# Performance work log

Hardware: AMD Instinct MI355X
Metric: run time of the kernel (lower is better)

Reference implementation:

```python
import jax, jax.numpy as jnp
import numpy as np

B, S, D, H = 4, 2048, 1024, 16
DK = D // H
THETA = 10000.0


def apply_rope(x, pos, theta):
    # x: [B, H, S, DK], pos: [S] int
    d = x.shape[-1]
    inv_freq = theta ** (-jnp.arange(0, d, 2, dtype=jnp.float32) / d)  # [d/2]
    ang = pos.astype(jnp.float32)[:, None] * inv_freq[None, :]          # [S, d/2]
    cos, sin = jnp.cos(ang), jnp.sin(ang)
    x1 = x[..., 0::2]
    x2 = x[..., 1::2]
    r1 = x1 * cos - x2 * sin
    r2 = x1 * sin + x2 * cos
    return jnp.stack([r1, r2], axis=-1).reshape(x.shape)


def setup_inputs() -> dict:
    key = jax.random.key(0)
    ks = jax.random.split(key, 5)
    scale = 1.0 / np.sqrt(D)
    x = jax.random.normal(ks[0], (B, S, D), dtype=jnp.float32)
    Wq = jax.random.normal(ks[1], (D, D), dtype=jnp.float32) * scale
    Wk = jax.random.normal(ks[2], (D, D), dtype=jnp.float32) * scale
    Wv = jax.random.normal(ks[3], (D, D), dtype=jnp.float32) * scale
    Wo = jax.random.normal(ks[4], (D, D), dtype=jnp.float32) * scale
    token_positions = jnp.arange(S, dtype=jnp.int32)
    return {"x": x, "token_positions": token_positions,
            "Wq": Wq, "Wk": Wk, "Wv": Wv, "Wo": Wo}


def reference(x, token_positions, Wq, Wk, Wv, Wo):
    b, s, d = x.shape
    # Linear (no bias), weight stored [out, in]: y = x @ W.T
    q = (x @ Wq.T).reshape(b, s, H, DK).transpose(0, 2, 1, 3)  # [B,H,S,DK]
    k = (x @ Wk.T).reshape(b, s, H, DK).transpose(0, 2, 1, 3)
    v = (x @ Wv.T).reshape(b, s, H, DK).transpose(0, 2, 1, 3)
    q = apply_rope(q, token_positions, THETA)
    k = apply_rope(k, token_positions, THETA)
    scores = jnp.einsum('bhqd,bhkd->bhqk', q, k) / jnp.sqrt(jnp.float32(DK))
    causal = jnp.tril(jnp.ones((s, s), dtype=bool))
    scores = jnp.where(causal, scores, -jnp.inf)
    attn = jax.nn.softmax(scores, axis=-1)
    out = jnp.einsum('bhqk,bhkd->bhqd', attn, v)
    out = out.transpose(0, 2, 1, 3).reshape(b, s, d)
    return out @ Wo.T
```

## Files before the change

### kernel.cpp

```cpp
#include <hip/hip_runtime.h>

typedef unsigned short u16;
typedef __bf16 bf16x8 __attribute__((ext_vector_type(8)));
typedef float f32x4 __attribute__((ext_vector_type(4)));
typedef u16 u16x8 __attribute__((ext_vector_type(8)));
typedef u16 u16x4 __attribute__((ext_vector_type(4)));
typedef short s16x4 __attribute__((ext_vector_type(4)));

union V8 { u16x8 u; bf16x8 b; };
union V4 { u16x4 u; s16x4 s; unsigned w[2]; };

#define NB 4
#define NS 2048
#define ND 1024
#define NH 16
#define NDK 64
#define LP 80
#define CP 136
#define QSCL 0.18033688011112042f
#define FMAX 20.0f

__device__ __forceinline__ u16 f2bf(float f) {
  union { float f; unsigned u; } v; v.f = f;
  return (u16)((v.u + 0x7fffu + ((v.u >> 16) & 1u)) >> 16);
}

__device__ __forceinline__ unsigned pk2bf(float a, float b) {
#if __has_builtin(__builtin_amdgcn_cvt_pk_bf16_f32)
  auto v = __builtin_amdgcn_cvt_pk_bf16_f32(a, b);
  unsigned r; __builtin_memcpy(&r, &v, 4);
  return r;
#else
  return (unsigned)f2bf(a) | ((unsigned)f2bf(b) << 16);
#endif
}

__device__ __forceinline__ float fexp2(float x) {
#if __has_builtin(__builtin_amdgcn_exp2f)
  return __builtin_amdgcn_exp2f(x);
#else
  return exp2f(x);
#endif
}

__device__ __forceinline__ bf16x8 lds_frag(const u16* p) {
  V8 t; t.u = *(const u16x8*)p; return t.b;
}

__global__ __launch_bounds__(256) void cvt_bf16(const float* __restrict__ s,
                                                u16* __restrict__ d, int n) {
  const int i = (blockIdx.x * 256 + threadIdx.x) * 8;
  if (i >= n) return;
  const f32x4 lo = *(const f32x4*)(s + i);
  const f32x4 hi = *(const f32x4*)(s + i + 4);
  union { unsigned w[4]; u16x8 v; } o;
  o.w[0] = pk2bf(lo[0], lo[1]);
  o.w[1] = pk2bf(lo[2], lo[3]);
  o.w[2] = pk2bf(hi[0], hi[1]);
  o.w[3] = pk2bf(hi[2], hi[3]);
  *(u16x8*)(d + i) = o.v;
}

__global__ __launch_bounds__(256) void cvt_w4(const float* __restrict__ w0,
                                              const float* __restrict__ w1,
                                              const float* __restrict__ w2,
                                              const float* __restrict__ w3,
                                              u16* __restrict__ d) {
  const float* s = (blockIdx.y == 0) ? w0 : (blockIdx.y == 1) ? w1
                 : (blockIdx.y == 2) ? w2 : w3;
  const int i = (blockIdx.x * 256 + threadIdx.x) * 8;
  const f32x4 lo = *(const f32x4*)(s + i);
  const f32x4 hi = *(const f32x4*)(s + i + 4);
  union { unsigned w[4]; u16x8 v; } o;
  o.w[0] = pk2bf(lo[0], lo[1]);
  o.w[1] = pk2bf(lo[2], lo[3]);
  o.w[2] = pk2bf(hi[0], hi[1]);
  o.w[3] = pk2bf(hi[2], hi[3]);
  *(u16x8*)(d + (size_t)blockIdx.y * ND * ND + i) = o.v;
}

__global__ __launch_bounds__(256) void rope_tbl(const int* __restrict__ tp,
                                                float2* __restrict__ tbl) {
  const int i = blockIdx.x * 256 + threadIdx.x;
  const int s = i >> 5, d = i & 31;
  const float inv = __expf(-(float)d * 0.28782313662425572f);
  const float ang = (float)tp[s] * inv;
  float sn, cs;
  __sincosf(ang, &sn, &cs);
  tbl[i] = make_float2(cs, sn);
}

__global__ __launch_bounds__(256) void gemm_qkv(
    const u16* __restrict__ X, const u16* __restrict__ W0,
    const u16* __restrict__ W1, const u16* __restrict__ W2,
    void* __restrict__ O0, void* __restrict__ O1, void* __restrict__ O2,
    const float2* __restrict__ tbl, int modebase) {
  __shared__ u16 smem[2 * 128 * LP];
  u16* ldsA = smem;
  u16* ldsB = smem + 128 * LP;
  const int tid = threadIdx.x;
  const int lane = tid & 63;
  const int w = tid >> 6;
  const int quad = lane >> 4;
  const int l15 = lane & 15;
  const int z = blockIdx.z;
  const u16* Wp = (z == 0) ? W0 : (z == 1) ? W1 : W2;
  void* Op = (z == 0) ? O0 : (z == 1) ? O1 : O2;
  const int mode = modebase + z;
  const int m0 = blockIdx.x * 128;
  const int n0 = blockIdx.y * 128;
  const int wm = (w >> 1) * 64;
  const int wn = (w & 1) * 64;

  const int srow = tid >> 3;
  const int scol = (tid & 7) * 8;
  const u16* Ag = X + (size_t)(m0 + srow) * ND + scol;
  const u16* Bg = Wp + (size_t)(n0 + srow) * ND + scol;

  f32x4 acc[4][4];
  const f32x4 z4 = {0.f, 0.f, 0.f, 0.f};
  for (int i = 0; i < 4; i++)
    for (int j = 0; j < 4; j++) acc[i][j] = z4;

  for (int k0 = 0; k0 < ND; k0 += 64) {
    u16x8 ar[4], br[4];
    for (int r = 0; r < 4; r++) {
      ar[r] = *(const u16x8*)(Ag + (size_t)r * 32 * ND + k0);
      br[r] = *(const u16x8*)(Bg + (size_t)r * 32 * ND + k0);
    }
    __syncthreads();
    for (int r = 0; r < 4; r++) {
      *(u16x8*)&ldsA[(r * 32 + srow) * LP + scol] = ar[r];
      *(u16x8*)&ldsB[(r * 32 + srow) * LP + scol] = br[r];
    }
    __syncthreads();
    for (int kk = 0; kk < 2; kk++) {
      bf16x8 af[4], bfr[4];
      for (int mt = 0; mt < 4; mt++)
        af[mt] = lds_frag(&ldsA[(wm + mt * 16 + l15) * LP + (kk * 4 + quad) * 8]);
      for (int nt = 0; nt < 4; nt++)
        bfr[nt] = lds_frag(&ldsB[(wn + nt * 16 + l15) * LP + (kk * 4 + quad) * 8]);
      for (int mt = 0; mt < 4; mt++)
        for (int nt = 0; nt < 4; nt++)
          acc[mt][nt] = __builtin_amdgcn_mfma_f32_16x16x32_bf16(
              af[mt], bfr[nt], acc[mt][nt], 0, 0, 0);
    }
  }
  __syncthreads();

  if (mode < 2) {
    u16* cb = smem;
    for (int nt = 0; nt < 4; nt++) {
      const int n_g = n0 + wn + nt * 16 + l15;
      const int dk = n_g & 63;
      const float sgn = (dk & 1) ? 1.f : -1.f;
      const int d2 = dk >> 1;
      for (int mt = 0; mt < 4; mt++) {
        const int mrow = wm + mt * 16 + quad * 4;
        for (int r = 0; r < 4; r++) {
          const int m_g = m0 + mrow + r;
          float v = acc[mt][nt][r];
          const int s_i = m_g & (NS - 1);
          const float partner = __shfl_xor(v, 1);
          const float2 t = tbl[s_i * 32 + d2];
          v = v * t.x + partner * t.y * sgn;
          if (mode == 0) v *= QSCL;
          cb[(mrow + r) * CP + wn + nt * 16 + l15] = f2bf(v);
        }
      }
    }
    __syncthreads();
    const int c = (tid & 15) * 8;
    const int h = (n0 + c) >> 6;
    const int dk0 = (n0 + c) & 63;
    for (int p = 0; p < 8; p++) {
      const int row = p * 16 + (tid >> 4);
      const int m_g = m0 + row;
      const int b = m_g >> 11;
      const int s_i = m_g & (NS - 1);
      *(u16x8*)&((u16*)Op)[(size_t)(((b * NH) + h) * NS + s_i) * NDK + dk0] =
          *(const u16x8*)&cb[row * CP + c];
    }
  } else if (mode == 2) {
    u16* cbT = smem;
    for (int nt = 0; nt < 4; nt++)
      for (int mt = 0; mt < 4; mt++)
        for (int r = 0; r < 4; r++)
          cbT[(wn + nt * 16 + l15) * CP + wm + mt * 16 + quad * 4 + r] =
              f2bf(acc[mt][nt][r]);
    __syncthreads();
    const int b = m0 >> 11;
    const int s0 = m0 & (NS - 1);
    const int col = (tid & 15) * 8;
    for (int p = 0; p < 8; p++) {
      const int row = p * 16 + (tid >> 4);
      const int dkg = n0 + row;
      const int h = dkg >> 6;
      *(u16x8*)&((u16*)Op)[(size_t)(((b * NH) + h) * NDK + (dkg & 63)) * NS +
                           s0 + col] = *(const u16x8*)&cbT[row * CP + col];
    }
  } else {
    for (int nt = 0; nt < 4; nt++) {
      const int n_g = n0 + wn + nt * 16 + l15;
      for (int mt = 0; mt < 4; mt++) {
        const int mb = m0 + wm + mt * 16 + quad * 4;
        for (int r = 0; r < 4; r++)
          ((float*)Op)[(size_t)(mb + r) * ND + n_g] = acc[mt][nt][r];
      }
    }
  }
}

__global__ __launch_bounds__(512, 4) void attn(const u16* __restrict__ Q,
                                               const u16* __restrict__ Kc,
                                               const u16* __restrict__ Vt,
                                               u16* __restrict__ AO,
                                               unsigned* __restrict__ ctr) {
  __shared__ u16 smem[2 * 64 * LP];
  u16* kt = smem;
  u16* vt = smem + 64 * LP;
  __shared__ unsigned s_item;
  const int tid = threadIdx.x;
  const int lane = tid & 63;
  const int w = tid >> 6;
  const int quad = lane >> 4;
  const int l15 = lane & 15;

  if (tid == 0) s_item = atomicAdd(ctr, 1u) & 1023u;
  __syncthreads();
  const unsigned item = s_item;
  const int qt = 15 - (int)(item >> 6);
  const int bh = (int)(item & 63u);
  const int q0 = qt * 128;
  const int qg = q0 + w * 16 + l15;
  const int qmin = q0 + w * 16;

  const int x7 = l15 & 7;
  const int kb0 = l15 * LP + ((quad ^ x7) * 8);
  const int kb1 = l15 * LP + (((4 + quad) ^ x7) * 8);
  int vb[4];
#pragma unroll
  for (int nt = 0; nt < 4; nt++)
    vb[nt] = l15 * LP + (((2 * nt + (quad >> 1)) ^ x7) * 8) + 4 * (quad & 1);
  const int srow = tid >> 3;
  const int sg = tid & 7;
  const int woff = srow * LP + ((sg ^ (srow & 7)) * 8);

  const u16* Qb = Q + (size_t)bh * NS * NDK + (size_t)qg * NDK + quad * 8;
  const bf16x8 qf0 = lds_frag(Qb);
  const bf16x8 qf1 = lds_frag(Qb + 32);

  f32x4 oacc[4];
  const f32x4 z4 = {0.f, 0.f, 0.f, 0.f};
#pragma unroll
  for (int i = 0; i < 4; i++) oacc[i] = z4;
  float ls0 = 0.f, ls1 = 0.f;

  const u16* Kb = Kc + (size_t)bh * NS * NDK;
  const u16* Vg = Vt + (size_t)bh * NDK * NS;

  u16x8 kreg = *(const u16x8*)(Kb + (size_t)srow * NDK + sg * 8);
  u16x8 vreg = *(const u16x8*)(Vg + (size_t)srow * NS + sg * 8);

  const int jend = q0 + 64;
  const f32x4 nF = {-FMAX, -FMAX, -FMAX, -FMAX};
  for (int j0 = 0; j0 <= jend; j0 += 64) {
    __syncthreads();
    *(u16x8*)&kt[woff] = kreg;
    *(u16x8*)&vt[woff] = vreg;
    __syncthreads();
    if (j0 + 64 <= jend) {
      const int nj = j0 + 64;
      kreg = *(const u16x8*)(Kb + (size_t)(nj + srow) * NDK + sg * 8);
      vreg = *(const u16x8*)(Vg + (size_t)srow * NS + nj + sg * 8);
    }

    if (j0 <= qmin + 15) {
      f32x4 sa[4];
#pragma unroll
      for (int i = 0; i < 4; i++) sa[i] = nF;
      __builtin_amdgcn_s_setprio(1);
#pragma unroll
      for (int nt = 0; nt < 4; nt++) {
        const bf16x8 kf0 = lds_frag(&kt[kb0 + nt * (16 * LP)]);
        sa[nt] = __builtin_amdgcn_mfma_f32_16x16x32_bf16(kf0, qf0, sa[nt], 0, 0, 0);
      }
#pragma unroll
      for (int nt = 0; nt < 4; nt++) {
        const bf16x8 kf1 = lds_frag(&kt[kb1 + nt * (16 * LP)]);
        sa[nt] = __builtin_amdgcn_mfma_f32_16x16x32_bf16(kf1, qf1, sa[nt], 0, 0, 0);
      }
      __builtin_amdgcn_s_setprio(0);

      const bool domask = (j0 + 63 > qmin);
      s16x4 pa[4];
#pragma unroll
      for (int nt = 0; nt < 4; nt++) {
        float p0 = fexp2(sa[nt][0]);
        float p1 = fexp2(sa[nt][1]);
        float p2 = fexp2(sa[nt][2]);
        float p3 = fexp2(sa[nt][3]);
        if (domask) {
          const int kbase = j0 + nt * 16 + quad * 4;
          if (kbase + 0 > qg) p0 = 0.f;
          if (kbase + 1 > qg) p1 = 0.f;
          if (kbase + 2 > qg) p2 = 0.f;
          if (kbase + 3 > qg) p3 = 0.f;
        }
        ls0 += p0 + p1;
        ls1 += p2 + p3;
        V4 t;
        t.w[0] = pk2bf(p0, p1);
        t.w[1] = pk2bf(p2, p3);
        pa[nt] = t.s;
      }

      __builtin_amdgcn_s_setprio(1);
#pragma unroll
      for (int dt = 0; dt < 4; dt++) {
#pragma unroll
        for (int nt = 0; nt < 4; nt++) {
          V4 t;
          t.u = *(const u16x4*)&vt[vb[nt] + dt * (16 * LP)];
          oacc[dt] = __builtin_amdgcn_mfma_f32_16x16x16bf16_1k(pa[nt], t.s,
                                                               oacc[dt], 0, 0, 0);
        }
      }
      __builtin_amdgcn_s_setprio(0);
    }
  }

  float lsum = ls0 + ls1;
  lsum += __shfl_xor(lsum, 16);
  lsum += __shfl_xor(lsum, 32);
  float lq[4];
#pragma unroll
  for (int r = 0; r < 4; r++) lq[r] = __shfl(lsum, quad * 4 + r);

  __syncthreads();
  u16* ob = smem;
#pragma unroll
  for (int dt = 0; dt < 4; dt++)
#pragma unroll
    for (int r = 0; r < 4; r++)
      ob[(w * 16 + quad * 4 + r) * 72 + dt * 16 + l15] =
          f2bf(oacc[dt][r] / lq[r]);
  __syncthreads();
  const int b = bh >> 4, h = bh & 15;
#pragma unroll
  for (int p2 = 0; p2 < 2; p2++) {
    const int idx = p2 * 512 + tid;
    const int row = idx >> 3;
    const int c = (idx & 7) * 8;
    *(u16x8*)&AO[(size_t)(b * NS + q0 + row) * ND + h * 64 + c] =
        *(const u16x8*)&ob[row * 72 + c];
  }
}

extern "C" void kernel_launch(void* const* d_in, const int* in_sizes, int n_in,
                              void* d_out, int out_size, void* d_ws, size_t ws_size,
                              hipStream_t stream) {
  const float* x = (const float*)d_in[0];
  const int* tp = (const int*)d_in[1];
  const float* Wq = (const float*)d_in[2];
  const float* Wk = (const float*)d_in[3];
  const float* Wv = (const float*)d_in[4];
  const float* Wo = (const float*)d_in[5];

  const size_t NE = (size_t)NB * NS * ND;
  const int NW = ND * ND;
  u16* Qb = (u16*)d_ws;
  u16* Kb = Qb + NE;
  u16* Vtb = Kb + NE;
  u16* Xbf = Vtb + NE;
  u16* Wbf = Xbf + NE;
  u16* wend = Wbf + 4 * (size_t)NW;
  unsigned* ctr = (unsigned*)wend;
  float2* tbl = (float2*)(wend + 8);

  dim3 blk(256);
  cvt_bf16<<<dim3((unsigned)(NE / 2048)), blk, 0, stream>>>(x, Xbf, (int)NE);
  cvt_w4<<<dim3(NW / 2048, 4), blk, 0, stream>>>(Wq, Wk, Wv, Wo, Wbf);
  rope_tbl<<<dim3(256), blk, 0, stream>>>(tp, tbl);
  gemm_qkv<<<dim3(64, 8, 3), blk, 0, stream>>>(
      Xbf, Wbf, Wbf + (size_t)NW, Wbf + 2 * (size_t)NW, Qb, Kb, Vtb, tbl, 0);
  attn<<<dim3(1024), dim3(512), 0, stream>>>(Qb, Kb, Vtb, Xbf, ctr);
  gemm_qkv<<<dim3(64, 8, 1), blk, 0, stream>>>(
      Xbf, Wbf + 3 * (size_t)NW, Wbf + 3 * (size_t)NW, Wbf + 3 * (size_t)NW,
      d_out, d_out, d_out, tbl, 3);
}
```

Measured before the change: 281.9 us.

## Shrink attention blocks to 64-query tiles and drop atomic work counter

The attention kernel now uses 256-thread blocks handling 64 queries each (4 waves) instead of 512 threads and 128 queries. The grid doubles to 2048, and blocks take their tile from blockIdx in heaviest-first order instead of an atomic counter. Each thread now loads two rows of the K/V tile. The per-wave causal skip goes away because the diagonal tile lines up with the block, so no wave idles on masked tiles. The cost is that each K/V tile is reused by fewer queries, so K/V traffic from global memory doubles, and scheduling order now depends on the hardware dispatcher rather than the atomic.

Result: slower. 434.4 us (+54.1%).

```diff
diff --git a/kernel.cpp b/kernel.cpp
--- a/kernel.cpp
+++ b/kernel.cpp
@@ -211,29 +211,24 @@
   }
 }
 
-__global__ __launch_bounds__(512, 4) void attn(const u16* __restrict__ Q,
+__global__ __launch_bounds__(256, 8) void attn(const u16* __restrict__ Q,
                                                const u16* __restrict__ Kc,
                                                const u16* __restrict__ Vt,
-                                               u16* __restrict__ AO,
-                                               unsigned* __restrict__ ctr) {
+                                               u16* __restrict__ AO) {
   __shared__ u16 smem[2 * 64 * LP];
   u16* kt = smem;
   u16* vt = smem + 64 * LP;
-  __shared__ unsigned s_item;
   const int tid = threadIdx.x;
   const int lane = tid & 63;
   const int w = tid >> 6;
   const int quad = lane >> 4;
   const int l15 = lane & 15;
 
-  if (tid == 0) s_item = atomicAdd(ctr, 1u) & 1023u;
-  __syncthreads();
-  const unsigned item = s_item;
-  const int qt = 15 - (int)(item >> 6);
-  const int bh = (int)(item & 63u);
-  const int q0 = qt * 128;
+  const int item = blockIdx.x;
+  const int qt = 31 - (item >> 6);
+  const int bh = item & 63;
+  const int q0 = qt * 64;
   const int qg = q0 + w * 16 + l15;
-  const int qmin = q0 + w * 16;
 
   const int x7 = l15 & 7;
   const int kb0 = l15 * LP + ((quad ^ x7) * 8);
@@ -244,7 +239,12 @@
     vb[nt] = l15 * LP + (((2 * nt + (quad >> 1)) ^ x7) * 8) + 4 * (quad & 1);
   const int srow = tid >> 3;
   const int sg = tid & 7;
-  const int woff = srow * LP + ((sg ^ (srow & 7)) * 8);
+  int woff[2];
+#pragma unroll
+  for (int r = 0; r < 2; r++) {
+    const int row = r * 32 + srow;
+    woff[r] = row * LP + ((sg ^ (row & 7)) * 8);
+  }
 
   const u16* Qb = Q + (size_t)bh * NS * NDK + (size_t)qg * NDK + quad * 8;
   const bf16x8 qf0 = lds_frag(Qb);
@@ -259,75 +259,84 @@
   const u16* Kb = Kc + (size_t)bh * NS * NDK;
   const u16* Vg = Vt + (size_t)bh * NDK * NS;
 
-  u16x8 kreg = *(const u16x8*)(Kb + (size_t)srow * NDK + sg * 8);
-  u16x8 vreg = *(const u16x8*)(Vg + (size_t)srow * NS + sg * 8);
-
-  const int jend = q0 + 64;
+  u16x8 kreg[2], vreg[2];
+#pragma unroll
+  for (int r = 0; r < 2; r++) {
+    const int row = r * 32 + srow;
+    kreg[r] = *(const u16x8*)(Kb + (size_t)row * NDK + sg * 8);
+    vreg[r] = *(const u16x8*)(Vg + (size_t)row * NS + sg * 8);
+  }
+
   const f32x4 nF = {-FMAX, -FMAX, -FMAX, -FMAX};
-  for (int j0 = 0; j0 <= jend; j0 += 64) {
-    __syncthreads();
-    *(u16x8*)&kt[woff] = kreg;
-    *(u16x8*)&vt[woff] = vreg;
-    __syncthreads();
-    if (j0 + 64 <= jend) {
+  for (int j0 = 0; j0 <= q0; j0 += 64) {
+    __syncthreads();
+#pragma unroll
+    for (int r = 0; r < 2; r++) {
+      *(u16x8*)&kt[woff[r]] = kreg[r];
+      *(u16x8*)&vt[woff[r]] = vreg[r];
+    }
+    __syncthreads();
+    if (j0 + 64 <= q0) {
       const int nj = j0 + 64;
-      kreg = *(const u16x8*)(Kb + (size_t)(nj + srow) * NDK + sg * 8);
-      vreg = *(const u16x8*)(Vg + (size_t)srow * NS + nj + sg * 8);
-    }
-
-    if (j0 <= qmin + 15) {
-      f32x4 sa[4];
-#pragma unroll
-      for (int i = 0; i < 4; i++) sa[i] = nF;
-      __builtin_amdgcn_s_setprio(1);
+#pragma unroll
+      for (int r = 0; r < 2; r++) {
+        const int row = r * 32 + srow;
+        kreg[r] = *(const u16x8*)(Kb + (size_t)(nj + row) * NDK + sg * 8);
+        vreg[r] = *(const u16x8*)(Vg + (size_t)row * NS + nj + sg * 8);
+      }
+    }
+
+    f32x4 sa[4];
+#pragma unroll
+    for (int i = 0; i < 4; i++) sa[i] = nF;
+    __builtin_amdgcn_s_setprio(1);
+#pragma unroll
+    for (int nt = 0; nt < 4; nt++) {
+      const bf16x8 kf0 = lds_frag(&kt[kb0 + nt * (16 * LP)]);
+      sa[nt] = __builtin_amdgcn_mfma_f32_16x16x32_bf16(kf0, qf0, sa[nt], 0, 0, 0);
+    }
+#pragma unroll
+    for (int nt = 0; nt < 4; nt++) {
+      const bf16x8 kf1 = lds_frag(&kt[kb1 + nt * (16 * LP)]);
+      sa[nt] = __builtin_amdgcn_mfma_f32_16x16x32_bf16(kf1, qf1, sa[nt], 0, 0, 0);
+    }
+    __builtin_amdgcn_s_setprio(0);
+
+    const bool domask = (j0 == q0);
+    s16x4 pa[4];
+#pragma unroll
+    for (int nt = 0; nt < 4; nt++) {
+      float p0 = fexp2(sa[nt][0]);
+      float p1 = fexp2(sa[nt][1]);
+      float p2 = fexp2(sa[nt][2]);
+      float p3 = fexp2(sa[nt][3]);
+      if (domask) {
+        const int kbase = j0 + nt * 16 + quad * 4;
+        if (kbase + 0 > qg) p0 = 0.f;
+        if (kbase + 1 > qg) p1 = 0.f;
+        if (kbase + 2 > qg) p2 = 0.f;
+        if (kbase + 3 > qg) p3 = 0.f;
+      }
+      ls0 += p0 + p1;
+      ls1 += p2 + p3;
+      V4 t;
+      t.w[0] = pk2bf(p0, p1);
+      t.w[1] = pk2bf(p2, p3);
+      pa[nt] = t.s;
+    }
+
+    __builtin_amdgcn_s_setprio(1);
+#pragma unroll
+    for (int dt = 0; dt < 4; dt++) {
 #pragma unroll
       for (int nt = 0; nt < 4; nt++) {
-        const bf16x8 kf0 = lds_frag(&kt[kb0 + nt * (16 * LP)]);
-        sa[nt] = __builtin_amdgcn_mfma_f32_16x16x32_bf16(kf0, qf0, sa[nt], 0, 0, 0);
-      }
-#pragma unroll
-      for (int nt = 0; nt < 4; nt++) {
-        const bf16x8 kf1 = lds_frag(&kt[kb1 + nt * (16 * LP)]);
-        sa[nt] = __builtin_amdgcn_mfma_f32_16x16x32_bf16(kf1, qf1, sa[nt], 0, 0, 0);
-      }
-      __builtin_amdgcn_s_setprio(0);
-
-      const bool domask = (j0 + 63 > qmin);
-      s16x4 pa[4];
-#pragma unroll
-      for (int nt = 0; nt < 4; nt++) {
-        float p0 = fexp2(sa[nt][0]);
-        float p1 = fexp2(sa[nt][1]);
-        float p2 = fexp2(sa[nt][2]);
-        float p3 = fexp2(sa[nt][3]);
-        if (domask) {
-          const int kbase = j0 + nt * 16 + quad * 4;
-          if (kbase + 0 > qg) p0 = 0.f;
-          if (kbase + 1 > qg) p1 = 0.f;
-          if (kbase + 2 > qg) p2 = 0.f;
-          if (kbase + 3 > qg) p3 = 0.f;
-        }
-        ls0 += p0 + p1;
-        ls1 += p2 + p3;
         V4 t;
-        t.w[0] = pk2bf(p0, p1);
-        t.w[1] = pk2bf(p2, p3);
-        pa[nt] = t.s;
-      }
-
-      __builtin_amdgcn_s_setprio(1);
-#pragma unroll
-      for (int dt = 0; dt < 4; dt++) {
-#pragma unroll
-        for (int nt = 0; nt < 4; nt++) {
-          V4 t;
-          t.u = *(const u16x4*)&vt[vb[nt] + dt * (16 * LP)];
-          oacc[dt] = __builtin_amdgcn_mfma_f32_16x16x16bf16_1k(pa[nt], t.s,
-                                                               oacc[dt], 0, 0, 0);
-        }
-      }
-      __builtin_amdgcn_s_setprio(0);
-    }
+        t.u = *(const u16x4*)&vt[vb[nt] + dt * (16 * LP)];
+        oacc[dt] = __builtin_amdgcn_mfma_f32_16x16x16bf16_1k(pa[nt], t.s,
+                                                             oacc[dt], 0, 0, 0);
+      }
+    }
+    __builtin_amdgcn_s_setprio(0);
   }
 
   float lsum = ls0 + ls1;
@@ -349,7 +358,7 @@
   const int b = bh >> 4, h = bh & 15;
 #pragma unroll
   for (int p2 = 0; p2 < 2; p2++) {
-    const int idx = p2 * 512 + tid;
+    const int idx = p2 * 256 + tid;
     const int row = idx >> 3;
     const int c = (idx & 7) * 8;
     *(u16x8*)&AO[(size_t)(b * NS + q0 + row) * ND + h * 64 + c] =
@@ -375,7 +384,6 @@
   u16* Xbf = Vtb + NE;
   u16* Wbf = Xbf + NE;
   u16* wend = Wbf + 4 * (size_t)NW;
-  unsigned* ctr = (unsigned*)wend;
   float2* tbl = (float2*)(wend + 8);
 
   dim3 blk(256);
@@ -384,7 +392,7 @@
   rope_tbl<<<dim3(256), blk, 0, stream>>>(tp, tbl);
   gemm_qkv<<<dim3(64, 8, 3), blk, 0, stream>>>(
       Xbf, Wbf, Wbf + (size_t)NW, Wbf + 2 * (size_t)NW, Qb, Kb, Vtb, tbl, 0);
-  attn<<<dim3(1024), dim3(512), 0, stream>>>(Qb, Kb, Vtb, Xbf, ctr);
+  attn<<<dim3(2048), blk, 0, stream>>>(Qb, Kb, Vtb, Xbf);
   gemm_qkv<<<dim3(64, 8, 1), blk, 0, stream>>>(
       Xbf, Wbf + 3 * (size_t)NW, Wbf + 3 * (size_t)NW, Wbf + 3 * (size_t)NW,
       d_out, d_out, d_out, tbl, 3);
```
